# Performance work log

Measured on AMD Instinct MI355X. Metric: run time of the kernel, lower is better.

The kernel has to match this reference:

```python
import jax, jax.numpy as jnp
import numpy as np

B, L, DIM, H, HD = 1, 2048, 2048, 16, 128  # head_dim = DIM // H; RoPE pairs = HD // 2


def setup_inputs() -> dict:
    key = jax.random.key(0)
    ks = jax.random.split(key, 6)
    x = jax.random.normal(ks[0], (B, L, DIM), dtype=jnp.float32)
    pe = jax.random.normal(ks[1], (1, 1, L, HD // 2, 2, 2), dtype=jnp.float32)
    qkv_w = jax.random.normal(ks[2], (3 * DIM, DIM), dtype=jnp.float32) * 0.02
    q_scale = jnp.ones((HD,), dtype=jnp.float32)
    k_scale = jnp.ones((HD,), dtype=jnp.float32)
    proj_w = jax.random.normal(ks[3], (DIM, DIM), dtype=jnp.float32) * 0.02
    proj_b = jnp.zeros((DIM,), dtype=jnp.float32)
    return {"x": x, "pe": pe, "qkv_w": qkv_w, "q_scale": q_scale,
            "k_scale": k_scale, "proj_w": proj_w, "proj_b": proj_b}


def _rmsnorm(t, scale):
    # per-head-dim RMSNorm, eps=1e-6, computed in fp32 (inputs already fp32)
    rrms = jax.lax.rsqrt(jnp.mean(t * t, axis=-1, keepdims=True) + 1e-6)
    return t * rrms * scale


def _apply_rope(q, k, pe):
    def rot(t):
        t_ = t.reshape(*t.shape[:-1], -1, 1, 2)  # [B,H,L,HD/2,1,2]
        out = pe[..., 0] * t_[..., 0] + pe[..., 1] * t_[..., 1]  # [B,H,L,HD/2,2]
        return out.reshape(t.shape)
    return rot(q), rot(k)


def reference(x, pe, qkv_w, q_scale, k_scale, proj_w, proj_b):
    b, l, _ = x.shape
    qkv = jnp.einsum('bld,ed->ble', x, qkv_w)  # [B, L, 3*DIM]
    qkv = qkv.reshape(b, l, 3, H, HD)
    # 'B L (K H D) -> K B H L D'
    qkv = jnp.transpose(qkv, (2, 0, 3, 1, 4))
    q, k, v = qkv[0], qkv[1], qkv[2]  # each [B, H, L, HD]
    q = _rmsnorm(q, q_scale)
    k = _rmsnorm(k, k_scale)
    q, k = _apply_rope(q, k, pe)
    scale = 1.0 / jnp.sqrt(jnp.asarray(HD, dtype=q.dtype))
    scores = jnp.einsum('bhqd,bhkd->bhqk', q, k) * scale
    attn = jax.nn.softmax(scores, axis=-1)
    out = jnp.einsum('bhqk,bhkd->bhqd', attn, v)  # [B, H, L, HD]
    out = jnp.transpose(out, (0, 2, 1, 3)).reshape(b, l, H * HD)  # 'B H L D -> B L (H D)'
    return jnp.einsum('bld,ed->ble', out, proj_w) + proj_b
```

## Files before the change

### kernel.cpp

```cpp
#include <hip/hip_runtime.h>
#include <hip/hip_bf16.h>
#include <math.h>

#define L_SEQ 2048
#define DIM   2048
#define NH    16
#define HD    128
#define TDIM  6144

typedef __attribute__((ext_vector_type(8))) short short8;
typedef __attribute__((ext_vector_type(4))) float f32x4;
typedef __attribute__((ext_vector_type(4))) unsigned int u32x4;

__device__ __forceinline__ void gl_lds16(const void* g, void* l) {
  __builtin_amdgcn_global_load_lds(
      (const __attribute__((address_space(1))) unsigned int*)g,
      (__attribute__((address_space(3))) unsigned int*)l, 16, 0, 0);
}

__device__ __forceinline__ short bf16bits(float x) {
  __hip_bfloat16 h = __float2bfloat16(x);
  return *(short*)&h;
}

__device__ __forceinline__ unsigned int pack_bf16(float a, float b) {
  __hip_bfloat162 h = __float22bfloat162_rn(make_float2(a, b));
  return *(unsigned int*)&h;
}

__global__ __launch_bounds__(256)
void cast_bf16(const float* __restrict__ in, __hip_bfloat16* __restrict__ out, int n) {
  int i = (blockIdx.x * 256 + threadIdx.x) * 8;
  if (i >= n) return;
  float4 a = *(const float4*)(in + i);
  float4 b = *(const float4*)(in + i + 4);
  short8 o;
  o[0] = bf16bits(a.x); o[1] = bf16bits(a.y); o[2] = bf16bits(a.z); o[3] = bf16bits(a.w);
  o[4] = bf16bits(b.x); o[5] = bf16bits(b.y); o[6] = bf16bits(b.z); o[7] = bf16bits(b.w);
  *(short8*)(out + i) = o;
}

template<int OUT_MODE>
__global__ __launch_bounds__(256)
void gemm_mfma(const __hip_bfloat16* __restrict__ A, const __hip_bfloat16* __restrict__ B,
               const float* __restrict__ bias, void* __restrict__ Cout,
               int M, int N, int K) {
  const int n0 = blockIdx.x * 128, m0 = blockIdx.y * 128;
  const int t = threadIdx.x, lane = t & 63, w = t >> 6;
  const int l15 = lane & 15, quad = lane >> 4;
  const int wm = (w & 1) * 64, wn = (w >> 1) * 64;

  __shared__ __align__(16) __hip_bfloat16 As[128 * 32];
  __shared__ __align__(16) __hip_bfloat16 Bs[128 * 32];

  f32x4 acc[4][4];
#pragma unroll
  for (int mt = 0; mt < 4; ++mt)
#pragma unroll
    for (int nt = 0; nt < 4; ++nt) acc[mt][nt] = (f32x4){0.f, 0.f, 0.f, 0.f};

  const int arow  = lane >> 2;
  const int acol8 = (lane & 3) * 8;
  const __hip_bfloat16* Ab = A + (size_t)(m0 + w * 16 + arow) * K + acol8;
  const __hip_bfloat16* Bb = B + (size_t)(n0 + w * 16 + arow) * K + acol8;
  __hip_bfloat16* As_base = As + (size_t)(w * 16) * 32;
  __hip_bfloat16* Bs_base = Bs + (size_t)(w * 16) * 32;

  for (int kb = 0; kb < K; kb += 32) {
    gl_lds16(Ab + kb,                As_base);
    gl_lds16(Ab + kb + (size_t)64*K, As_base + 64 * 32);
    gl_lds16(Bb + kb,                Bs_base);
    gl_lds16(Bb + kb + (size_t)64*K, Bs_base + 64 * 32);
    __syncthreads();

    short8 am[4], bn[4];
#pragma unroll
    for (int mt = 0; mt < 4; ++mt)
      am[mt] = *(const short8*)&As[(size_t)(wm + mt*16 + l15) * 32 + quad * 8];
#pragma unroll
    for (int nt = 0; nt < 4; ++nt)
      bn[nt] = *(const short8*)&Bs[(size_t)(wn + nt*16 + l15) * 32 + quad * 8];
#pragma unroll
    for (int mt = 0; mt < 4; ++mt)
#pragma unroll
      for (int nt = 0; nt < 4; ++nt)
        acc[mt][nt] = __builtin_amdgcn_mfma_f32_16x16x32_bf16(am[mt], bn[nt], acc[mt][nt], 0, 0, 0);
    __syncthreads();
  }

#pragma unroll
  for (int mt = 0; mt < 4; ++mt) {
#pragma unroll
    for (int nt = 0; nt < 4; ++nt) {
      int col = n0 + wn + nt * 16 + l15;
#pragma unroll
      for (int r = 0; r < 4; ++r) {
        int row = m0 + wm + mt * 16 + quad * 4 + r;
        if (OUT_MODE == 0) {
          ((__hip_bfloat16*)Cout)[(size_t)row * N + col] = __float2bfloat16(acc[mt][nt][r]);
        } else {
          ((float*)Cout)[(size_t)row * N + col] = acc[mt][nt][r] + bias[col];
        }
      }
    }
  }
}

__global__ __launch_bounds__(128)
void norm_rope(const __hip_bfloat16* __restrict__ qkv_b, const float* __restrict__ pe,
               const float* __restrict__ q_scale, const float* __restrict__ k_scale,
               __hip_bfloat16* __restrict__ Qb, __hip_bfloat16* __restrict__ Kb) {
  const int l  = blockIdx.x;
  const int hh = blockIdx.y;
  const int qk_sel = hh >> 4;
  const int h  = hh & 15;
  const int d  = threadIdx.x;
  const __hip_bfloat16* row = qkv_b + (size_t)l * TDIM + qk_sel * DIM + h * HD;
  const float* scale = qk_sel ? k_scale : q_scale;

  float v  = __bfloat162float(row[d]);
  float sq = v * v;
#pragma unroll
  for (int o = 32; o > 0; o >>= 1) sq += __shfl_xor(sq, o);
  __shared__ float wsum[2];
  if ((d & 63) == 0) wsum[d >> 6] = sq;
  __syncthreads();
  float rrms = rsqrtf((wsum[0] + wsum[1]) * (1.f / 128.f) + 1e-6f);
  __shared__ float nb[128];
  nb[d] = v * rrms * scale[d];
  __syncthreads();
  int i = d >> 1, c = d & 1;
  const float* p = pe + ((size_t)(l * 64 + i) * 2 + c) * 2;
  float res = p[0] * nb[2*i] + p[1] * nb[2*i + 1];
  size_t o_idx = ((size_t)h * L_SEQ + l) * HD + d;
  if (qk_sel == 0) Qb[o_idx] = __float2bfloat16(res * 0.08838834764831845f);
  else             Kb[o_idx] = __float2bfloat16(res);
}

__global__ __launch_bounds__(256)
void v_transpose(const __hip_bfloat16* __restrict__ qkv_b, __hip_bfloat16* __restrict__ Vt) {
  const int l0 = blockIdx.x * 64;
  const int h  = blockIdx.y;
  const int t  = threadIdx.x;
  __shared__ __align__(16) __hip_bfloat16 T[128][72];
#pragma unroll
  for (int it = 0; it < 4; ++it) {
    int idx = t + it * 256;
    int row = idx >> 4;
    int c8  = (idx & 15) * 8;
    short8 v = *(const short8*)&qkv_b[(size_t)(l0 + row) * TDIM + 2 * DIM + h * HD + c8];
#pragma unroll
    for (int j = 0; j < 8; ++j) *(short*)&T[c8 + j][row] = v[j];
  }
  __syncthreads();
#pragma unroll
  for (int it = 0; it < 4; ++it) {
    int idx = t + it * 256;
    int d = idx >> 3, c8 = (idx & 7) * 8;
    *(short8*)(Vt + ((size_t)h * HD + d) * L_SEQ + l0 + c8) = *(const short8*)&T[d][c8];
  }
}

__global__ __launch_bounds__(256, 2)
void attn_mfma(const __hip_bfloat16* __restrict__ Qb,
               const __hip_bfloat16* __restrict__ Kb,
               const __hip_bfloat16* __restrict__ Vt,
               __hip_bfloat16* __restrict__ out) {
  const int q0 = blockIdx.x * 64;
  const int h  = blockIdx.y;
  const int t  = threadIdx.x;
  const int lane = t & 63, w = t >> 6;
  const int l15 = lane & 15, quad = lane >> 4;
  const int sw = l15 & 7;

  __shared__ __align__(16) __hip_bfloat16 Ks[2][64 * 128];
  __shared__ __align__(16) __hip_bfloat16 Vs[2][128 * 64];

  const __hip_bfloat16* kbase = Kb + (size_t)h * L_SEQ * HD;
  const __hip_bfloat16* vbase = Vt + (size_t)h * HD * L_SEQ;

  short8 aq[4];
  {
    const __hip_bfloat16* qbase = Qb + ((size_t)h * L_SEQ + q0 + w * 16 + l15) * HD;
#pragma unroll
    for (int ks = 0; ks < 4; ++ks)
      aq[ks] = *(const short8*)(qbase + ks * 32 + quad * 8);
  }

  f32x4 o[8];
#pragma unroll
  for (int n2 = 0; n2 < 8; ++n2) o[n2] = (f32x4){0.f, 0.f, 0.f, 0.f};
  float m_run = -1e30f, l_run = 0.f;

#define STAGE(buf, k0)                                                          \
  {                                                                             \
    _Pragma("unroll")                                                           \
    for (int i = 0; i < 4; ++i) {                                               \
      int krow = w * 16 + i * 4 + (lane >> 4);                                  \
      int kch  = (lane & 15) ^ (krow & 7);                                      \
      gl_lds16(kbase + (size_t)((k0) + krow) * HD + kch * 8,                    \
               &Ks[buf][(w * 16 + i * 4) * 128]);                               \
    }                                                                           \
    _Pragma("unroll")                                                           \
    for (int i = 0; i < 4; ++i) {                                               \
      int vrow = w * 32 + i * 8 + (lane >> 3);                                  \
      int vch  = (lane & 7) ^ (vrow & 7);                                       \
      gl_lds16(vbase + (size_t)vrow * L_SEQ + (k0) + vch * 8,                   \
               &Vs[buf][(w * 32 + i * 8) * 64]);                                \
    }                                                                           \
  }

  STAGE(0, 0);
  __syncthreads();

  for (int kt = 0; kt < L_SEQ / 64; ++kt) {
    const int cur = kt & 1;
    if (kt + 1 < L_SEQ / 64) STAGE(cur ^ 1, (kt + 1) * 64);

    f32x4 s[4];
#pragma unroll
    for (int nt = 0; nt < 4; ++nt) s[nt] = (f32x4){0.f, 0.f, 0.f, 0.f};
#pragma unroll
    for (int ks = 0; ks < 4; ++ks) {
      short8 bk[4];
#pragma unroll
      for (int nt = 0; nt < 4; ++nt)
        bk[nt] = *(const short8*)&Ks[cur][(nt * 16 + l15) * 128 + ((ks * 4 + quad) ^ sw) * 8];
#pragma unroll
      for (int nt = 0; nt < 4; ++nt)
        s[nt] = __builtin_amdgcn_mfma_f32_16x16x32_bf16(bk[nt], aq[ks], s[nt], 0, 0, 0);
    }

    float mx0 = fmaxf(fmaxf(s[0][0], s[0][1]), fmaxf(s[0][2], s[0][3]));
    float mx1 = fmaxf(fmaxf(s[1][0], s[1][1]), fmaxf(s[1][2], s[1][3]));
    float mx2 = fmaxf(fmaxf(s[2][0], s[2][1]), fmaxf(s[2][2], s[2][3]));
    float mx3 = fmaxf(fmaxf(s[3][0], s[3][1]), fmaxf(s[3][2], s[3][3]));
    float rm = fmaxf(fmaxf(mx0, mx1), fmaxf(mx2, mx3));
    rm = fmaxf(rm, __shfl_xor(rm, 16));
    rm = fmaxf(rm, __shfl_xor(rm, 32));
    float mnew = fmaxf(m_run, rm);
    float alpha = __expf(m_run - mnew);
    m_run = mnew;

    float sum = 0.f;
#pragma unroll
    for (int nt = 0; nt < 4; ++nt)
#pragma unroll
      for (int r = 0; r < 4; ++r) {
        float p = __expf(s[nt][r] - mnew);
        s[nt][r] = p;
        sum += p;
      }
    sum += __shfl_xor(sum, 16);
    sum += __shfl_xor(sum, 32);
    l_run = l_run * alpha + sum;

    float alpha_r[4];
#pragma unroll
    for (int r = 0; r < 4; ++r) alpha_r[r] = __shfl(alpha, quad * 4 + r);
#pragma unroll
    for (int n2 = 0; n2 < 8; ++n2)
#pragma unroll
      for (int r = 0; r < 4; ++r) o[n2][r] *= alpha_r[r];

    unsigned int pk[4][2];
#pragma unroll
    for (int nt = 0; nt < 4; ++nt) {
      pk[nt][0] = pack_bf16(s[nt][0], s[nt][1]);
      pk[nt][1] = pack_bf16(s[nt][2], s[nt][3]);
    }
    short8 ap[2];
#pragma unroll
    for (int ks2 = 0; ks2 < 2; ++ks2) {
      u32x4 a32;
#pragma unroll
      for (int jp = 0; jp < 4; ++jp) {
        int quad_src = (quad & 1) * 2 + (jp >> 1);
        int src = (quad_src << 4) | l15;
        int rp = jp & 1;
        unsigned int v0 = __shfl((int)pk[2 * ks2 + 0][rp], src);
        unsigned int v1 = __shfl((int)pk[2 * ks2 + 1][rp], src);
        a32[jp] = (quad >> 1) ? v1 : v0;
      }
      ap[ks2] = *(short8*)&a32;
    }

#pragma unroll
    for (int ks2 = 0; ks2 < 2; ++ks2)
#pragma unroll
      for (int n2 = 0; n2 < 8; ++n2) {
        short8 bv = *(const short8*)&Vs[cur][(n2 * 16 + l15) * 64 + ((ks2 * 4 + quad) ^ sw) * 8];
        o[n2] = __builtin_amdgcn_mfma_f32_16x16x32_bf16(ap[ks2], bv, o[n2], 0, 0, 0);
      }

    __syncthreads();
  }

  float linv[4];
#pragma unroll
  for (int r = 0; r < 4; ++r) linv[r] = 1.f / __shfl(l_run, quad * 4 + r);
#pragma unroll
  for (int r = 0; r < 4; ++r) {
    int q = q0 + w * 16 + quad * 4 + r;
#pragma unroll
    for (int n2 = 0; n2 < 8; ++n2)
      out[(size_t)q * DIM + h * HD + n2 * 16 + l15] = __float2bfloat16(o[n2][r] * linv[r]);
  }
#undef STAGE
}

extern "C" void kernel_launch(void* const* d_in, const int* in_sizes, int n_in,
                              void* d_out, int out_size, void* d_ws, size_t ws_size,
                              hipStream_t stream) {
  const float* x       = (const float*)d_in[0];
  const float* pe      = (const float*)d_in[1];
  const float* qkv_w   = (const float*)d_in[2];
  const float* q_scale = (const float*)d_in[3];
  const float* k_scale = (const float*)d_in[4];
  const float* proj_w  = (const float*)d_in[5];
  const float* proj_b  = (const float*)d_in[6];
  float* out = (float*)d_out;

  char* base = (char*)d_ws;
  __hip_bfloat16* wb       = (__hip_bfloat16*)base;
  __hip_bfloat16* qkv_b    = (__hip_bfloat16*)(base + 25165824);
  __hip_bfloat16* xb       = (__hip_bfloat16*)(base + 50331648);
  __hip_bfloat16* Qb       = (__hip_bfloat16*)base;
  __hip_bfloat16* Kb       = (__hip_bfloat16*)(base + 8388608);
  __hip_bfloat16* Vt       = (__hip_bfloat16*)(base + 16777216);
  __hip_bfloat16* pwb      = (__hip_bfloat16*)(base + 25165824);
  __hip_bfloat16* attn_out = (__hip_bfloat16*)(base + 50331648);

  cast_bf16<<<dim3(DIM * DIM / (256 * 8)), 256, 0, stream>>>(x, xb, DIM * DIM);
  cast_bf16<<<dim3(TDIM * DIM / (256 * 8)), 256, 0, stream>>>(qkv_w, wb, TDIM * DIM);

  gemm_mfma<0><<<dim3(TDIM / 128, L_SEQ / 128), 256, 0, stream>>>(
      xb, wb, nullptr, qkv_b, L_SEQ, TDIM, DIM);

  norm_rope<<<dim3(L_SEQ, 2 * NH), 128, 0, stream>>>(qkv_b, pe, q_scale, k_scale, Qb, Kb);
  v_transpose<<<dim3(L_SEQ / 64, NH), 256, 0, stream>>>(qkv_b, Vt);

  cast_bf16<<<dim3(DIM * DIM / (256 * 8)), 256, 0, stream>>>(proj_w, pwb, DIM * DIM);

  attn_mfma<<<dim3(L_SEQ / 64, NH), 256, 0, stream>>>(Qb, Kb, Vt, attn_out);

  gemm_mfma<1><<<dim3(DIM / 128, DIM / 128), 256, 0, stream>>>(
      attn_out, pwb, proj_b, out, L_SEQ, DIM, DIM);
}
```

Measured before the change: 341.9 us.

## Split attention over two KV halves with combine kernel; single-buffer LDS; fuse casts

The attention kernel is split along the key dimension into two halves (grid z=2). Each half writes a normalized bf16 partial output plus its running max and sum, and a new combine kernel merges the halves with softmax rescaling. LDS drops to a single buffer and launch bounds rise to 4 blocks per CU, giving more occupancy and parallelism at the cost of the earlier prefetch overlap. The x and qkv_w casts are merged into one launch. Costs are an extra kernel, extra global traffic for the partials, and bf16 rounding of the partials.

```diff
diff --git a/kernel.cpp b/kernel.cpp
--- a/kernel.cpp
+++ b/kernel.cpp
@@ -23,9 +23,31 @@
   return *(short*)&h;
 }
 
+__device__ __forceinline__ float bits2f(short s) {
+  unsigned int u = ((unsigned int)(unsigned short)s) << 16;
+  return __uint_as_float(u);
+}
+
 __device__ __forceinline__ unsigned int pack_bf16(float a, float b) {
   __hip_bfloat162 h = __float22bfloat162_rn(make_float2(a, b));
   return *(unsigned int*)&h;
+}
+
+__global__ __launch_bounds__(256)
+void cast2_bf16(const float* __restrict__ a, __hip_bfloat16* __restrict__ oa,
+                const float* __restrict__ b, __hip_bfloat16* __restrict__ ob) {
+  int i = (blockIdx.x * 256 + threadIdx.x) * 8;
+  const float* src;
+  __hip_bfloat16* dst;
+  int off;
+  if (i < DIM * DIM) { src = a; dst = oa; off = i; }
+  else               { src = b; dst = ob; off = i - DIM * DIM; }
+  float4 v0 = *(const float4*)(src + off);
+  float4 v1 = *(const float4*)(src + off + 4);
+  short8 o;
+  o[0] = bf16bits(v0.x); o[1] = bf16bits(v0.y); o[2] = bf16bits(v0.z); o[3] = bf16bits(v0.w);
+  o[4] = bf16bits(v1.x); o[5] = bf16bits(v1.y); o[6] = bf16bits(v1.z); o[7] = bf16bits(v1.w);
+  *(short8*)(dst + off) = o;
 }
 
 __global__ __launch_bounds__(256)
@@ -161,20 +183,21 @@
   }
 }
 
-__global__ __launch_bounds__(256, 2)
+__global__ __launch_bounds__(256, 4)
 void attn_mfma(const __hip_bfloat16* __restrict__ Qb,
                const __hip_bfloat16* __restrict__ Kb,
                const __hip_bfloat16* __restrict__ Vt,
-               __hip_bfloat16* __restrict__ out) {
+               __hip_bfloat16* __restrict__ Opart, float2* __restrict__ ml) {
   const int q0 = blockIdx.x * 64;
   const int h  = blockIdx.y;
+  const int z  = blockIdx.z;
   const int t  = threadIdx.x;
   const int lane = t & 63, w = t >> 6;
   const int l15 = lane & 15, quad = lane >> 4;
   const int sw = l15 & 7;
 
-  __shared__ __align__(16) __hip_bfloat16 Ks[2][64 * 128];
-  __shared__ __align__(16) __hip_bfloat16 Vs[2][128 * 64];
+  __shared__ __align__(16) __hip_bfloat16 Ks[64 * 128];
+  __shared__ __align__(16) __hip_bfloat16 Vs[128 * 64];
 
   const __hip_bfloat16* kbase = Kb + (size_t)h * L_SEQ * HD;
   const __hip_bfloat16* vbase = Vt + (size_t)h * HD * L_SEQ;
@@ -192,30 +215,23 @@
   for (int n2 = 0; n2 < 8; ++n2) o[n2] = (f32x4){0.f, 0.f, 0.f, 0.f};
   float m_run = -1e30f, l_run = 0.f;
 
-#define STAGE(buf, k0)                                                          \
-  {                                                                             \
-    _Pragma("unroll")                                                           \
-    for (int i = 0; i < 4; ++i) {                                               \
-      int krow = w * 16 + i * 4 + (lane >> 4);                                  \
-      int kch  = (lane & 15) ^ (krow & 7);                                      \
-      gl_lds16(kbase + (size_t)((k0) + krow) * HD + kch * 8,                    \
-               &Ks[buf][(w * 16 + i * 4) * 128]);                               \
-    }                                                                           \
-    _Pragma("unroll")                                                           \
-    for (int i = 0; i < 4; ++i) {                                               \
-      int vrow = w * 32 + i * 8 + (lane >> 3);                                  \
-      int vch  = (lane & 7) ^ (vrow & 7);                                       \
-      gl_lds16(vbase + (size_t)vrow * L_SEQ + (k0) + vch * 8,                   \
-               &Vs[buf][(w * 32 + i * 8) * 64]);                                \
-    }                                                                           \
-  }
-
-  STAGE(0, 0);
-  __syncthreads();
-
-  for (int kt = 0; kt < L_SEQ / 64; ++kt) {
-    const int cur = kt & 1;
-    if (kt + 1 < L_SEQ / 64) STAGE(cur ^ 1, (kt + 1) * 64);
+  for (int kt = 0; kt < 16; ++kt) {
+    const int k0 = z * (L_SEQ / 2) + kt * 64;
+#pragma unroll
+    for (int i = 0; i < 4; ++i) {
+      int krow = w * 16 + i * 4 + (lane >> 4);
+      int kch  = (lane & 15) ^ (krow & 7);
+      gl_lds16(kbase + (size_t)(k0 + krow) * HD + kch * 8,
+               &Ks[(w * 16 + i * 4) * 128]);
+    }
+#pragma unroll
+    for (int i = 0; i < 4; ++i) {
+      int vrow = w * 32 + i * 8 + (lane >> 3);
+      int vch  = (lane & 7) ^ (vrow & 7);
+      gl_lds16(vbase + (size_t)vrow * L_SEQ + k0 + vch * 8,
+               &Vs[(w * 32 + i * 8) * 64]);
+    }
+    __syncthreads();
 
     f32x4 s[4];
 #pragma unroll
@@ -225,7 +241,7 @@
       short8 bk[4];
 #pragma unroll
       for (int nt = 0; nt < 4; ++nt)
-        bk[nt] = *(const short8*)&Ks[cur][(nt * 16 + l15) * 128 + ((ks * 4 + quad) ^ sw) * 8];
+        bk[nt] = *(const short8*)&Ks[(nt * 16 + l15) * 128 + ((ks * 4 + quad) ^ sw) * 8];
 #pragma unroll
       for (int nt = 0; nt < 4; ++nt)
         s[nt] = __builtin_amdgcn_mfma_f32_16x16x32_bf16(bk[nt], aq[ks], s[nt], 0, 0, 0);
@@ -289,24 +305,49 @@
     for (int ks2 = 0; ks2 < 2; ++ks2)
 #pragma unroll
       for (int n2 = 0; n2 < 8; ++n2) {
-        short8 bv = *(const short8*)&Vs[cur][(n2 * 16 + l15) * 64 + ((ks2 * 4 + quad) ^ sw) * 8];
+        short8 bv = *(const short8*)&Vs[(n2 * 16 + l15) * 64 + ((ks2 * 4 + quad) ^ sw) * 8];
         o[n2] = __builtin_amdgcn_mfma_f32_16x16x32_bf16(ap[ks2], bv, o[n2], 0, 0, 0);
       }
 
     __syncthreads();
   }
 
+  const size_t rb = (size_t)(z * NH + h) * L_SEQ + q0 + w * 16;
   float linv[4];
 #pragma unroll
   for (int r = 0; r < 4; ++r) linv[r] = 1.f / __shfl(l_run, quad * 4 + r);
 #pragma unroll
   for (int r = 0; r < 4; ++r) {
-    int q = q0 + w * 16 + quad * 4 + r;
+    size_t row = rb + quad * 4 + r;
 #pragma unroll
     for (int n2 = 0; n2 < 8; ++n2)
-      out[(size_t)q * DIM + h * HD + n2 * 16 + l15] = __float2bfloat16(o[n2][r] * linv[r]);
-  }
-#undef STAGE
+      Opart[row * HD + n2 * 16 + l15] = __float2bfloat16(o[n2][r] * linv[r]);
+  }
+  if (quad == 0) ml[rb + l15] = make_float2(m_run, l_run);
+}
+
+__global__ __launch_bounds__(256)
+void attn_combine(const __hip_bfloat16* __restrict__ Opart,
+                  const float2* __restrict__ ml,
+                  __hip_bfloat16* __restrict__ out) {
+  const int h  = blockIdx.y;
+  const int q  = blockIdx.x * 16 + (threadIdx.x >> 4);
+  const int d8 = (threadIdx.x & 15) * 8;
+  const size_t i0 = (size_t)h * L_SEQ + q;
+  const size_t i1 = (size_t)(NH + h) * L_SEQ + q;
+  float2 a = ml[i0], b = ml[i1];
+  float M  = fmaxf(a.x, b.x);
+  float w1 = __expf(a.x - M) * a.y;
+  float w2 = __expf(b.x - M) * b.y;
+  float inv = 1.f / (w1 + w2);
+  w1 *= inv; w2 *= inv;
+  short8 o1 = *(const short8*)&Opart[i0 * HD + d8];
+  short8 o2 = *(const short8*)&Opart[i1 * HD + d8];
+  short8 r;
+#pragma unroll
+  for (int j = 0; j < 8; ++j)
+    r[j] = bf16bits(w1 * bits2f(o1[j]) + w2 * bits2f(o2[j]));
+  *(short8*)&out[(size_t)q * DIM + h * HD + d8] = r;
 }
 
 extern "C" void kernel_launch(void* const* d_in, const int* in_sizes, int n_in,
@@ -329,10 +370,12 @@
   __hip_bfloat16* Kb       = (__hip_bfloat16*)(base + 8388608);
   __hip_bfloat16* Vt       = (__hip_bfloat16*)(base + 16777216);
   __hip_bfloat16* pwb      = (__hip_bfloat16*)(base + 25165824);
-  __hip_bfloat16* attn_out = (__hip_bfloat16*)(base + 50331648);
-
-  cast_bf16<<<dim3(DIM * DIM / (256 * 8)), 256, 0, stream>>>(x, xb, DIM * DIM);
-  cast_bf16<<<dim3(TDIM * DIM / (256 * 8)), 256, 0, stream>>>(qkv_w, wb, TDIM * DIM);
+  __hip_bfloat16* Opart    = (__hip_bfloat16*)(base + 33554432);
+  float2*         ml       = (float2*)(base + 50331648);
+  __hip_bfloat16* attn_out = (__hip_bfloat16*)base;
+
+  cast2_bf16<<<dim3((DIM * DIM + TDIM * DIM) / (256 * 8)), 256, 0, stream>>>(
+      x, xb, qkv_w, wb);
 
   gemm_mfma<0><<<dim3(TDIM / 128, L_SEQ / 128), 256, 0, stream>>>(
       xb, wb, nullptr, qkv_b, L_SEQ, TDIM, DIM);
@@ -342,7 +385,8 @@
 
   cast_bf16<<<dim3(DIM * DIM / (256 * 8)), 256, 0, stream>>>(proj_w, pwb, DIM * DIM);
 
-  attn_mfma<<<dim3(L_SEQ / 64, NH), 256, 0, stream>>>(Qb, Kb, Vt, attn_out);
+  attn_mfma<<<dim3(L_SEQ / 64, NH, 2), 256, 0, stream>>>(Qb, Kb, Vt, Opart, ml);
+  attn_combine<<<dim3(L_SEQ / 16, NH), 256, 0, stream>>>(Opart, ml, attn_out);
 
   gemm_mfma<1><<<dim3(DIM / 128, DIM / 128), 256, 0, stream>>>(
       attn_out, pwb, proj_b, out, L_SEQ, DIM, DIM);
```

After: 343.0 us. No clear change (+0.3%).
